# Optimization experiments

Hardware: AMD Instinct MI355X
Metric: run time of the kernel (lower is better)

The kernel has to match this reference:

```python
import jax, jax.numpy as jnp
import numpy as np

PS = 32
D = 256


def setup_inputs() -> dict:
    key = jax.random.key(0)
    ks = jax.random.split(key, 9)
    B, L = 32, 32768
    s_in = 1.0 / np.sqrt(PS)
    s_d = 1.0 / np.sqrt(D)
    return {
        "x": jax.random.normal(ks[0], (B, L), dtype=jnp.float32),
        "W_proj": jax.random.normal(ks[1], (PS, D), dtype=jnp.float32) * s_in,
        "b_proj": jnp.zeros((D,), jnp.float32),
        "W_qkv": jax.random.normal(ks[2], (D, 3 * D), dtype=jnp.float32) * s_d,
        "b_qkv": jnp.zeros((3 * D,), jnp.float32),
        "W_out": jax.random.normal(ks[3], (D, D), dtype=jnp.float32) * s_d,
        "b_out": jnp.zeros((D,), jnp.float32),
        "W_head": jax.random.normal(ks[4], (D, PS), dtype=jnp.float32) * s_d,
        "b_head": jnp.zeros((PS,), jnp.float32),
    }


def reference(x, W_proj, b_proj, W_qkv, b_qkv, W_out, b_out, W_head, b_head):
    B, L = x.shape
    T = L // PS
    # InstanceNorm over full series (torch .std is unbiased -> ddof=1)
    mean = jnp.mean(x, axis=-1, keepdims=True)
    std = jnp.std(x, axis=-1, keepdims=True, ddof=1) + 1e-5
    x_norm = (x - mean) / std
    patches = x_norm.reshape(B, T, PS)
    # Patch embedding
    h = patches @ W_proj + b_proj  # [B, T, D]
    # Single-head causal self-attention (explicit scores, as in source)
    qkv = h @ W_qkv + b_qkv
    q, k, v = jnp.split(qkv, 3, axis=-1)
    scale = 1.0 / jnp.sqrt(jnp.asarray(D, dtype=h.dtype))
    attn = jnp.einsum("btd,bsd->bts", q, k) * scale  # [B, T, T]
    causal = jnp.tril(jnp.ones((T, T), dtype=bool))
    attn = jnp.where(causal, attn, -jnp.inf)
    attn = jax.nn.softmax(attn, axis=-1)
    out = jnp.einsum("bts,bsd->btd", attn, v)
    out = out @ W_out + b_out
    # Prediction head + next-patch MSE loss
    pred = out @ W_head + b_head  # [B, T, PS]
    loss = jnp.mean((pred[:, :-1] - patches[:, 1:]) ** 2)
    return loss
```

## Files before the change

kernel.cpp:

```cpp
#include <hip/hip_runtime.h>
#include <math.h>

#define B_SZ 32
#define L_SZ 32768
#define T_SZ 1024
#define PS_SZ 32
#define D_SZ 256
#define SM_M 10.0f

typedef float f32x4 __attribute__((ext_vector_type(4)));
typedef float f32x16 __attribute__((ext_vector_type(16)));
typedef short s16x8 __attribute__((ext_vector_type(8)));
typedef unsigned short u16x8 __attribute__((ext_vector_type(8)));
typedef unsigned int u32;
typedef unsigned int u32x4 __attribute__((ext_vector_type(4)));

__device__ __forceinline__ unsigned short f2bf(float f) {
  union { float f; unsigned int u; } v; v.f = f;
  unsigned int r = v.u + 0x7FFFu + ((v.u >> 16) & 1u);
  return (unsigned short)(r >> 16);
}

__device__ __forceinline__ void g2l16(const unsigned short* g, unsigned short* l) {
  __builtin_amdgcn_global_load_lds(
      (const __attribute__((address_space(1))) unsigned int*)g,
      (__attribute__((address_space(3))) unsigned int*)l, 16, 0, 0);
}

__global__ __launch_bounds__(256) void prep_kernel(const float* __restrict__ x,
                                                   float* __restrict__ sgpart,
                                                   const float* __restrict__ Wp,
                                                   const float* __restrict__ bp,
                                                   const float* __restrict__ Wq,
                                                   const float* __restrict__ bq,
                                                   const float* __restrict__ Wo,
                                                   const float* __restrict__ bo,
                                                   const float* __restrict__ Wh,
                                                   const float* __restrict__ bh,
                                                   float* __restrict__ Wcb,
                                                   unsigned short* __restrict__ WqT,
                                                   unsigned short* __restrict__ WfT,
                                                   float* __restrict__ bfp,
                                                   unsigned int* __restrict__ total,
                                                   float* __restrict__ lsum) {
  __shared__ float red[8];
  const int g = blockIdx.x, tid = threadIdx.x;
  const int w = tid >> 6, lane = tid & 63;
  if (g < 256) {
    const int b = g >> 3;
    const float* p = x + (size_t)b * L_SZ + (size_t)(g & 7) * 4096;
    float s = 0.f, ss = 0.f;
#pragma unroll
    for (int i = 0; i < 4; ++i) {
      float4 f = ((const float4*)p)[tid + i * 256];
      s += f.x + f.y + f.z + f.w;
      ss += f.x * f.x + f.y * f.y + f.z * f.z + f.w * f.w;
    }
#pragma unroll
    for (int off = 32; off >= 1; off >>= 1) {
      s += __shfl_down(s, off);
      ss += __shfl_down(ss, off);
    }
    if (lane == 0) { red[w] = s; red[4 + w] = ss; }
    __syncthreads();
    if (tid == 0) {
      sgpart[g * 2]     = red[0] + red[1] + red[2] + red[3];
      sgpart[g * 2 + 1] = red[4] + red[5] + red[6] + red[7];
    }
  } else if (g < 388) {
    int idx = (g - 256) * 256 + tid;
    if (idx < 33 * 768) {
      int p = idx / 768, j = idx % 768;
      const float* arow = (p < 32) ? (Wp + p * 256) : bp;
      float acc = (p < 32) ? 0.f : bq[j];
      for (int d = 0; d < 256; ++d) acc += arow[d] * Wq[d * 768 + j];
      if (p < 32) WqT[j * 32 + p] = f2bf(acc);
      else Wcb[j] = acc;
    } else {
      int k = idx - 33 * 768;
      if (k < 8192) {
        int p = k >> 8, d = k & 255;
        float acc = 0.f;
        for (int e = 0; e < 256; ++e) acc += Wo[d * 256 + e] * Wh[e * 32 + p];
        WfT[p * 256 + d] = f2bf(acc);
      } else if (k < 8224) {
        int p = k - 8192;
        float acc = bh[p];
        for (int e = 0; e < 256; ++e) acc += bo[e] * Wh[e * 32 + p];
        bfp[p] = acc;
      }
    }
  } else {
    if (tid == 0) { total[0] = 0u; lsum[0] = 0.f; }
  }
}

__global__ __launch_bounds__(256) void qkv_kernel(const float* __restrict__ x,
                                                  const float* __restrict__ sgpart,
                                                  const unsigned short* __restrict__ WqT,
                                                  const float* __restrict__ Wcb,
                                                  unsigned short* __restrict__ Qb,
                                                  unsigned short* __restrict__ Kb,
                                                  unsigned short* __restrict__ Vtt) {
  __shared__ unsigned short T4[4][8448];
  const int tid = threadIdx.x;
  const int w = tid >> 6, lane = tid & 63;
  const int lo = lane & 15, quad = lane >> 4;
  unsigned short* Tw = T4[w];
  const int mbase = blockIdx.x * 128 + w * 32;
  const int b = mbase >> 10;
  float S = 0.f, SS = 0.f;
#pragma unroll
  for (int i = 0; i < 8; ++i) {
    S += sgpart[(b * 8 + i) * 2];
    SS += sgpart[(b * 8 + i) * 2 + 1];
  }
  const float mean = S * (1.f / (float)L_SZ);
  const float var = (SS - S * mean) * (1.f / (float)(L_SZ - 1));
  const float inv = 1.f / (sqrtf(var) + 1e-5f);
  s16x8 af0, af1;
  {
    float4 a = *(const float4*)&x[(size_t)(mbase + lo) * 32 + quad * 8];
    float4 c = *(const float4*)&x[(size_t)(mbase + lo) * 32 + quad * 8 + 4];
    af0[0] = (short)f2bf((a.x - mean) * inv); af0[1] = (short)f2bf((a.y - mean) * inv);
    af0[2] = (short)f2bf((a.z - mean) * inv); af0[3] = (short)f2bf((a.w - mean) * inv);
    af0[4] = (short)f2bf((c.x - mean) * inv); af0[5] = (short)f2bf((c.y - mean) * inv);
    af0[6] = (short)f2bf((c.z - mean) * inv); af0[7] = (short)f2bf((c.w - mean) * inv);
    float4 d = *(const float4*)&x[(size_t)(mbase + 16 + lo) * 32 + quad * 8];
    float4 e = *(const float4*)&x[(size_t)(mbase + 16 + lo) * 32 + quad * 8 + 4];
    af1[0] = (short)f2bf((d.x - mean) * inv); af1[1] = (short)f2bf((d.y - mean) * inv);
    af1[2] = (short)f2bf((d.z - mean) * inv); af1[3] = (short)f2bf((d.w - mean) * inv);
    af1[4] = (short)f2bf((e.x - mean) * inv); af1[5] = (short)f2bf((e.y - mean) * inv);
    af1[6] = (short)f2bf((e.z - mean) * inv); af1[7] = (short)f2bf((e.w - mean) * inv);
  }
#pragma unroll 4
  for (int nt = 0; nt < 16; ++nt) {
    s16x8 bf = *(const s16x8*)&WqT[(size_t)(nt * 16 + lo) * 32 + quad * 8];
    f32x4 c0 = {0.f, 0.f, 0.f, 0.f}, c1 = {0.f, 0.f, 0.f, 0.f};
    c0 = __builtin_amdgcn_mfma_f32_16x16x32_bf16(af0, bf, c0, 0, 0, 0);
    c1 = __builtin_amdgcn_mfma_f32_16x16x32_bf16(af1, bf, c1, 0, 0, 0);
    const int col = nt * 16 + lo;
    const float bi = Wcb[col];
#pragma unroll
    for (int i = 0; i < 4; ++i) {
      Tw[(quad * 4 + i) * 264 + col]      = f2bf((c0[i] + bi) * 0.0625f);
      Tw[(16 + quad * 4 + i) * 264 + col] = f2bf((c1[i] + bi) * 0.0625f);
    }
  }
#pragma unroll
  for (int it = 0; it < 16; ++it) {
    const int gsub = it * 64 + lane;
    const int row = gsub >> 5, c16 = gsub & 31;
    *(u16x8*)&Qb[(size_t)(mbase + row) * 256 + c16 * 8] =
        *(const u16x8*)&Tw[row * 264 + c16 * 8];
  }
#pragma unroll 4
  for (int nt = 0; nt < 16; ++nt) {
    s16x8 bf = *(const s16x8*)&WqT[(size_t)(256 + nt * 16 + lo) * 32 + quad * 8];
    f32x4 c0 = {0.f, 0.f, 0.f, 0.f}, c1 = {0.f, 0.f, 0.f, 0.f};
    c0 = __builtin_amdgcn_mfma_f32_16x16x32_bf16(af0, bf, c0, 0, 0, 0);
    c1 = __builtin_amdgcn_mfma_f32_16x16x32_bf16(af1, bf, c1, 0, 0, 0);
    const int col = nt * 16 + lo;
    const float bi = Wcb[256 + col];
#pragma unroll
    for (int i = 0; i < 4; ++i) {
      Tw[(quad * 4 + i) * 264 + col]      = f2bf(c0[i] + bi);
      Tw[(16 + quad * 4 + i) * 264 + col] = f2bf(c1[i] + bi);
    }
  }
#pragma unroll
  for (int it = 0; it < 16; ++it) {
    const int gsub = it * 64 + lane;
    const int row = gsub >> 5, c16 = gsub & 31;
    *(u16x8*)&Kb[(size_t)(mbase + row) * 256 + c16 * 8] =
        *(const u16x8*)&Tw[row * 264 + c16 * 8];
  }
#pragma unroll 4
  for (int nt2 = 0; nt2 < 16; ++nt2) {
    s16x8 aw = *(const s16x8*)&WqT[(size_t)(512 + nt2 * 16 + lo) * 32 + quad * 8];
    f32x4 c0 = {0.f, 0.f, 0.f, 0.f}, c1 = {0.f, 0.f, 0.f, 0.f};
    c0 = __builtin_amdgcn_mfma_f32_16x16x32_bf16(aw, af0, c0, 0, 0, 0);
    c1 = __builtin_amdgcn_mfma_f32_16x16x32_bf16(aw, af1, c1, 0, 0, 0);
#pragma unroll
    for (int i = 0; i < 4; ++i) {
      const int d = nt2 * 16 + quad * 4 + i;
      const float bv = Wcb[512 + d];
      Tw[d * 32 + lo]      = f2bf(c0[i] + bv);
      Tw[d * 32 + 16 + lo] = f2bf(c1[i] + bv);
    }
  }
  {
    const int ktq = (mbase >> 5) & 31;
    const size_t vb = ((size_t)b * 32 + ktq) * 8192;
#pragma unroll
    for (int it = 0; it < 16; ++it) {
      const int gsub = it * 64 + lane;
      *(u16x8*)&Vtt[vb + gsub * 8] = *(const u16x8*)&Tw[gsub * 8];
    }
  }
}

__global__ __launch_bounds__(512, 2) void attn_kernel(const unsigned short* __restrict__ Qb,
                                                      const unsigned short* __restrict__ Kb,
                                                      const unsigned short* __restrict__ Vtt,
                                                      const unsigned short* __restrict__ WfT,
                                                      const float* __restrict__ bfp,
                                                      const float* __restrict__ x,
                                                      const float* __restrict__ sgpart,
                                                      float* __restrict__ lsum,
                                                      unsigned int* __restrict__ total,
                                                      float* __restrict__ out) {
  __shared__ unsigned short SMEM[65536];
  __shared__ float redf[8];
  const int g = blockIdx.x;
  const int b = (g & 7) * 4 + ((g >> 3) & 3);
  const int p = g >> 5;
  const int tid = threadIdx.x;
  const int w = tid >> 6, lane = tid & 63;
  const int th = w & 1, dq = w >> 1;
  const int cl = lane & 31, hi = lane >> 5;

  const unsigned short* KbB = Kb + (size_t)b * 262144;
  const unsigned short* VtB = Vtt + (size_t)b * 262144;
  unsigned short* QbM = (unsigned short*)Qb;

  const int c0 = tid, c1 = 512 + tid;
  const int ks0 = (c0 >> 5) * 256 + (((c0 & 31) ^ (c0 >> 5)) * 8);
  const int ks1 = (c1 >> 5) * 256 + (((c1 & 31) ^ (c1 >> 5)) * 8);
  const int vs0 = (c0 >> 2) * 32 + (((c0 & 3) ^ ((c0 >> 4) & 3)) * 8);
  const int vs1 = (c1 >> 2) * 32 + (((c1 & 3) ^ ((c1 >> 4) & 3)) * 8);
  const int kd0 = w * 512, kd1 = 4096 + w * 512;

  auto STAGE = [&](int t) {
    const unsigned short* kg = KbB + (size_t)t * 8192;
    const unsigned short* vg = VtB + (size_t)t * 8192;
    unsigned short* Lb = &SMEM[(t & 3) * 16384];
    g2l16(kg + ks0, Lb + kd0);
    g2l16(kg + ks1, Lb + kd1);
    g2l16(vg + vs0, Lb + 8192 + kd0);
    g2l16(vg + vs1, Lb + 8192 + kd1);
  };

  s16x8 qf[16];
  f32x16 O0, O1;
  float Ol = 0.f;
  const int vsz = (cl >> 2) & 3;
  const int cva = (hi ^ vsz) * 8, cvb = (((2 | hi)) ^ vsz) * 8;

  auto run_phase = [&](int gph) {
    const int nk = 2 * gph + 2;
    const int myti = 2 * gph + th;
    const size_t qrow = ((size_t)b * 1024 + myti * 32 + cl) * 256;
#pragma unroll
    for (int cb = 0; cb < 16; ++cb) qf[cb] = *(const s16x8*)&Qb[qrow + cb * 16 + hi * 8];
#pragma unroll
    for (int i = 0; i < 16; ++i) { O0[i] = 0.f; O1[i] = 0.f; }
    Ol = 0.f;
    const int npre = nk < 3 ? nk : 3;
    for (int s = 0; s < npre; ++s) STAGE(s);
    for (int s = 0; s < nk; ++s) {
      const int rem = nk - 1 - s;
      if (rem >= 2)      asm volatile("s_waitcnt vmcnt(8)" ::: "memory");
      else if (rem == 1) asm volatile("s_waitcnt vmcnt(4)" ::: "memory");
      else               asm volatile("s_waitcnt vmcnt(0)" ::: "memory");
      __builtin_amdgcn_s_barrier();
      __builtin_amdgcn_sched_barrier(0);
      if (s + 3 < nk) STAGE(s + 3);
      if (s <= myti) {
        const unsigned short* Lk = &SMEM[(s & 3) * 16384];
        f32x16 Sx;
#pragma unroll
        for (int i = 0; i < 16; ++i) Sx[i] = 0.f;
#pragma unroll
        for (int cb = 0; cb < 16; ++cb) {
          const int ch = (2 * cb + hi) ^ cl;
          s16x8 kf = *(const s16x8*)&Lk[cl * 256 + ch * 8];
          Sx = __builtin_amdgcn_mfma_f32_32x32x16_bf16(kf, qf[cb], Sx, 0, 0, 0);
        }
        float e[16];
        const bool diag = (s == myti);
#pragma unroll
        for (int r = 0; r < 16; ++r) {
          const int trow = (r & 3) + 8 * (r >> 2) + 4 * hi;
          float ev = __expf(Sx[r] - SM_M);
          if (diag && trow > cl) ev = 0.f;
          e[r] = ev;
          Ol += ev;
        }
        u32 w8[8];
#pragma unroll
        for (int m = 0; m < 8; ++m)
          w8[m] = (u32)f2bf(e[2 * m]) | ((u32)f2bf(e[2 * m + 1]) << 16);
        const u32 r1 = (u32)__shfl_xor((int)(hi ? w8[0] : w8[2]), 32);
        const u32 r2 = (u32)__shfl_xor((int)(hi ? w8[1] : w8[3]), 32);
        const u32 r3 = (u32)__shfl_xor((int)(hi ? w8[4] : w8[6]), 32);
        const u32 r4 = (u32)__shfl_xor((int)(hi ? w8[5] : w8[7]), 32);
        union { u32x4 u; s16x8 s; } p0, p1;
        p0.u[0] = hi ? r1 : w8[0];
        p0.u[1] = hi ? r2 : w8[1];
        p0.u[2] = hi ? w8[2] : r1;
        p0.u[3] = hi ? w8[3] : r2;
        p1.u[0] = hi ? r3 : w8[4];
        p1.u[1] = hi ? r4 : w8[5];
        p1.u[2] = hi ? w8[6] : r3;
        p1.u[3] = hi ? w8[7] : r4;
        const unsigned short* Lv = &SMEM[(s & 3) * 16384 + 8192];
        const int d0 = (dq * 64 + cl) * 32, d1 = (dq * 64 + 32 + cl) * 32;
        s16x8 v0 = *(const s16x8*)&Lv[d0 + cva];
        s16x8 v1 = *(const s16x8*)&Lv[d0 + cvb];
        O0 = __builtin_amdgcn_mfma_f32_32x32x16_bf16(p0.s, v0, O0, 0, 0, 0);
        O0 = __builtin_amdgcn_mfma_f32_32x32x16_bf16(p1.s, v1, O0, 0, 0, 0);
        s16x8 v2 = *(const s16x8*)&Lv[d1 + cva];
        s16x8 v3 = *(const s16x8*)&Lv[d1 + cvb];
        O1 = __builtin_amdgcn_mfma_f32_32x32x16_bf16(p0.s, v2, O1, 0, 0, 0);
        O1 = __builtin_amdgcn_mfma_f32_32x32x16_bf16(p1.s, v3, O1, 0, 0, 0);
      }
    }
    Ol += __shfl_xor(Ol, 32);
  };

  run_phase(p);
  {
    float ivr[16];
#pragma unroll
    for (int r = 0; r < 16; ++r) {
      const int row = (r & 3) + 8 * (r >> 2) + 4 * hi;
      ivr[r] = 1.f / __shfl(Ol, row);
    }
    const size_t obase = ((size_t)b * 1024 + (2 * p + th) * 32) * 256;
#pragma unroll
    for (int r = 0; r < 16; ++r) {
      const int row = (r & 3) + 8 * (r >> 2) + 4 * hi;
      QbM[obase + row * 256 + dq * 64 + cl]      = f2bf(O0[r] * ivr[r]);
      QbM[obase + row * 256 + dq * 64 + 32 + cl] = f2bf(O1[r] * ivr[r]);
    }
  }
  asm volatile("s_waitcnt vmcnt(0)" ::: "memory");
  __builtin_amdgcn_s_barrier();

  run_phase(15 - p);
  __syncthreads();

  unsigned short* OLs = SMEM;
  {
    float ivr[16];
#pragma unroll
    for (int r = 0; r < 16; ++r) {
      const int row = (r & 3) + 8 * (r >> 2) + 4 * hi;
      ivr[r] = 1.f / __shfl(Ol, row);
    }
#pragma unroll
    for (int r = 0; r < 16; ++r) {
      const int row = (r & 3) + 8 * (r >> 2) + 4 * hi;
      OLs[(th * 32 + row) * 264 + dq * 64 + cl]      = f2bf(O0[r] * ivr[r]);
      OLs[(th * 32 + row) * 264 + dq * 64 + 32 + cl] = f2bf(O1[r] * ivr[r]);
    }
  }
  __syncthreads();

  float lacc = 0.f;
  if (w < 4) {
    const int tile = (w == 0) ? 2 * p : (w == 1) ? 2 * p + 1
                   : (w == 2) ? 30 - 2 * p : 31 - 2 * p;
    s16x8 af[16];
    if (w < 2) {
      const size_t abase = ((size_t)b * 1024 + tile * 32 + cl) * 256;
#pragma unroll
      for (int cb = 0; cb < 16; ++cb)
        af[cb] = *(const s16x8*)&QbM[abase + cb * 16 + hi * 8];
    } else {
      const int sub = w - 2;
#pragma unroll
      for (int cb = 0; cb < 16; ++cb)
        af[cb] = *(const s16x8*)&OLs[(sub * 32 + cl) * 264 + cb * 16 + hi * 8];
    }
    f32x16 hacc;
#pragma unroll
    for (int i = 0; i < 16; ++i) hacc[i] = 0.f;
#pragma unroll
    for (int cb = 0; cb < 16; ++cb) {
      s16x8 bfr = *(const s16x8*)&WfT[(size_t)cl * 256 + cb * 16 + hi * 8];
      hacc = __builtin_amdgcn_mfma_f32_32x32x16_bf16(af[cb], bfr, hacc, 0, 0, 0);
    }
    float S_ = 0.f, SS = 0.f;
#pragma unroll
    for (int i = 0; i < 8; ++i) {
      S_ += sgpart[(b * 8 + i) * 2];
      SS += sgpart[(b * 8 + i) * 2 + 1];
    }
    const float mean = S_ * (1.f / (float)L_SZ);
    const float var = (SS - S_ * mean) * (1.f / (float)(L_SZ - 1));
    const float invb = 1.f / (sqrtf(var) + 1e-5f);
    const float ba = bfp[cl];
#pragma unroll
    for (int r = 0; r < 16; ++r) {
      const int row = (r & 3) + 8 * (r >> 2) + 4 * hi;
      const int t = tile * 32 + row;
      if (t < 1023) {
        const float pr = hacc[r] + ba;
        const float tg = (x[(size_t)b * L_SZ + (t + 1) * 32 + cl] - mean) * invb;
        const float d = pr - tg;
        lacc += d * d;
      }
    }
#pragma unroll
    for (int off = 32; off >= 1; off >>= 1) lacc += __shfl_down(lacc, off);
  }
  if (lane == 0) redf[w] = lacc;
  __syncthreads();

  if (tid == 0) {
    atomicAdd(lsum, redf[0] + redf[1] + redf[2] + redf[3]);
    __threadfence();
    unsigned int prev = atomicAdd(total, 1u);
    if (prev == 255u) {
      float tot = atomicAdd(lsum, 0.0f);
      out[0] = tot * (1.f / (float)(B_SZ * (T_SZ - 1) * PS_SZ));
    }
  }
}

extern "C" void kernel_launch(void* const* d_in, const int* in_sizes, int n_in,
                              void* d_out, int out_size, void* d_ws, size_t ws_size,
                              hipStream_t stream) {
  const float* x      = (const float*)d_in[0];
  const float* W_proj = (const float*)d_in[1];
  const float* b_proj = (const float*)d_in[2];
  const float* W_qkv  = (const float*)d_in[3];
  const float* b_qkv  = (const float*)d_in[4];
  const float* W_out  = (const float*)d_in[5];
  const float* b_out  = (const float*)d_in[6];
  const float* W_head = (const float*)d_in[7];
  const float* b_head = (const float*)d_in[8];
  float* out = (float*)d_out;
  char* ws = (char*)d_ws;

  unsigned short* Qb     = (unsigned short*)ws;
  unsigned short* Kb     = (unsigned short*)(ws + (16ull << 20));
  unsigned short* Vtt    = (unsigned short*)(ws + (32ull << 20));
  char* tail = ws + (48ull << 20);
  float*          Wcb    = (float*)tail;
  unsigned short* WqT    = (unsigned short*)(tail + 4096);
  unsigned short* WfT    = (unsigned short*)(tail + 65536);
  float*          bfp    = (float*)(tail + 98304);
  float*          sgpart = (float*)(tail + 102400);
  unsigned int*   total  = (unsigned int*)(tail + 106496);
  float*          lsum   = (float*)(tail + 106496 + 64);

  prep_kernel<<<389, 256, 0, stream>>>(x, sgpart, W_proj, b_proj, W_qkv, b_qkv,
                                       W_out, b_out, W_head, b_head,
                                       Wcb, WqT, WfT, bfp, total, lsum);
  qkv_kernel<<<256, 256, 0, stream>>>(x, sgpart, WqT, Wcb, Qb, Kb, Vtt);
  attn_kernel<<<256, 512, 0, stream>>>(Qb, Kb, Vtt, WfT, bfp, x, sgpart, lsum, total, out);
}
```

Measured before the change: 181.2 us.

## Compute attention scores once per KV tile and share probabilities via LDS

```diff
diff --git a/kernel.cpp b/kernel.cpp
--- a/kernel.cpp
+++ b/kernel.cpp
@@ -13,6 +13,7 @@
 typedef short s16x8 __attribute__((ext_vector_type(8)));
 typedef unsigned short u16x8 __attribute__((ext_vector_type(8)));
 typedef unsigned int u32;
+typedef unsigned int u32x2 __attribute__((ext_vector_type(2)));
 typedef unsigned int u32x4 __attribute__((ext_vector_type(4)));
 
 __device__ __forceinline__ unsigned short f2bf(float f) {
@@ -211,13 +212,15 @@
                                                       unsigned int* __restrict__ total,
                                                       float* __restrict__ out) {
   __shared__ unsigned short SMEM[65536];
+  __shared__ unsigned short Pbuf[2][2][1280];
+  __shared__ float OlL[8][32];
   __shared__ float redf[8];
   const int g = blockIdx.x;
   const int b = (g & 7) * 4 + ((g >> 3) & 3);
   const int p = g >> 5;
   const int tid = threadIdx.x;
   const int w = tid >> 6, lane = tid & 63;
-  const int th = w & 1, dq = w >> 1;
+  const int th = w >> 2, dq = w & 3;
   const int cl = lane & 31, hi = lane >> 5;
 
   const unsigned short* KbB = Kb + (size_t)b * 262144;
@@ -245,115 +248,116 @@
   f32x16 O0, O1;
   float Ol = 0.f;
   const int vsz = (cl >> 2) & 3;
-  const int cva = (hi ^ vsz) * 8, cvb = (((2 | hi)) ^ vsz) * 8;
+  const int cva = (hi ^ vsz) * 8, cvb = ((2 | hi) ^ vsz) * 8;
+
+  auto PRODUCE = [&](int sp, int myti_) {
+    const unsigned short* Lk = &SMEM[(sp & 3) * 16384];
+    f32x16 Sx;
+#pragma unroll
+    for (int i = 0; i < 16; ++i) Sx[i] = 0.f;
+#pragma unroll
+    for (int cb = 0; cb < 16; ++cb) {
+      const int ch = (2 * cb + hi) ^ cl;
+      s16x8 kf = *(const s16x8*)&Lk[cl * 256 + ch * 8];
+      Sx = __builtin_amdgcn_mfma_f32_32x32x16_bf16(kf, qf[cb], Sx, 0, 0, 0);
+    }
+    const bool diag = (sp == myti_);
+    unsigned short* Pd = &Pbuf[th][sp & 1][0];
+#pragma unroll
+    for (int gq = 0; gq < 4; ++gq) {
+      float ev[4];
+#pragma unroll
+      for (int q2 = 0; q2 < 4; ++q2) {
+        const int r = gq * 4 + q2;
+        const int trow = q2 + 8 * gq + 4 * hi;
+        float e = __expf(Sx[r] - SM_M);
+        if (diag && trow > cl) e = 0.f;
+        ev[q2] = e;
+        Ol += e;
+      }
+      u32x2 pr;
+      pr[0] = (u32)f2bf(ev[0]) | ((u32)f2bf(ev[1]) << 16);
+      pr[1] = (u32)f2bf(ev[2]) | ((u32)f2bf(ev[3]) << 16);
+      *(u32x2*)&Pd[cl * 40 + (2 * gq + hi) * 4] = pr;
+    }
+  };
 
   auto run_phase = [&](int gph) {
     const int nk = 2 * gph + 2;
     const int myti = 2 * gph + th;
     const size_t qrow = ((size_t)b * 1024 + myti * 32 + cl) * 256;
 #pragma unroll
-    for (int cb = 0; cb < 16; ++cb) qf[cb] = *(const s16x8*)&Qb[qrow + cb * 16 + hi * 8];
+    for (int cb = 0; cb < 16; ++cb)
+      qf[cb] = *(const s16x8*)&Qb[qrow + cb * 16 + hi * 8];
 #pragma unroll
     for (int i = 0; i < 16; ++i) { O0[i] = 0.f; O1[i] = 0.f; }
     Ol = 0.f;
-    const int npre = nk < 3 ? nk : 3;
-    for (int s = 0; s < npre; ++s) STAGE(s);
+    if (nk >= 3) {
+      STAGE(0); STAGE(1); STAGE(2);
+      asm volatile("s_waitcnt vmcnt(8)" ::: "memory");
+    } else {
+      STAGE(0); STAGE(1);
+      asm volatile("s_waitcnt vmcnt(4)" ::: "memory");
+    }
+    __builtin_amdgcn_s_barrier();
+    if (w == th * 4 + ((2 * th) & 3)) PRODUCE(0, myti);
     for (int s = 0; s < nk; ++s) {
-      const int rem = nk - 1 - s;
-      if (rem >= 2)      asm volatile("s_waitcnt vmcnt(8)" ::: "memory");
-      else if (rem == 1) asm volatile("s_waitcnt vmcnt(4)" ::: "memory");
-      else               asm volatile("s_waitcnt vmcnt(0)" ::: "memory");
+      asm volatile("s_waitcnt lgkmcnt(0)" ::: "memory");
+      if (s + 2 < nk) asm volatile("s_waitcnt vmcnt(4)" ::: "memory");
+      else            asm volatile("s_waitcnt vmcnt(0)" ::: "memory");
       __builtin_amdgcn_s_barrier();
       __builtin_amdgcn_sched_barrier(0);
       if (s + 3 < nk) STAGE(s + 3);
+      if (s + 1 <= myti && w == th * 4 + ((s + 1 + 2 * th) & 3)) PRODUCE(s + 1, myti);
       if (s <= myti) {
-        const unsigned short* Lk = &SMEM[(s & 3) * 16384];
-        f32x16 Sx;
-#pragma unroll
-        for (int i = 0; i < 16; ++i) Sx[i] = 0.f;
-#pragma unroll
-        for (int cb = 0; cb < 16; ++cb) {
-          const int ch = (2 * cb + hi) ^ cl;
-          s16x8 kf = *(const s16x8*)&Lk[cl * 256 + ch * 8];
-          Sx = __builtin_amdgcn_mfma_f32_32x32x16_bf16(kf, qf[cb], Sx, 0, 0, 0);
-        }
-        float e[16];
-        const bool diag = (s == myti);
-#pragma unroll
-        for (int r = 0; r < 16; ++r) {
-          const int trow = (r & 3) + 8 * (r >> 2) + 4 * hi;
-          float ev = __expf(Sx[r] - SM_M);
-          if (diag && trow > cl) ev = 0.f;
-          e[r] = ev;
-          Ol += ev;
-        }
-        u32 w8[8];
-#pragma unroll
-        for (int m = 0; m < 8; ++m)
-          w8[m] = (u32)f2bf(e[2 * m]) | ((u32)f2bf(e[2 * m + 1]) << 16);
-        const u32 r1 = (u32)__shfl_xor((int)(hi ? w8[0] : w8[2]), 32);
-        const u32 r2 = (u32)__shfl_xor((int)(hi ? w8[1] : w8[3]), 32);
-        const u32 r3 = (u32)__shfl_xor((int)(hi ? w8[4] : w8[6]), 32);
-        const u32 r4 = (u32)__shfl_xor((int)(hi ? w8[5] : w8[7]), 32);
-        union { u32x4 u; s16x8 s; } p0, p1;
-        p0.u[0] = hi ? r1 : w8[0];
-        p0.u[1] = hi ? r2 : w8[1];
-        p0.u[2] = hi ? w8[2] : r1;
-        p0.u[3] = hi ? w8[3] : r2;
-        p1.u[0] = hi ? r3 : w8[4];
-        p1.u[1] = hi ? r4 : w8[5];
-        p1.u[2] = hi ? w8[6] : r3;
-        p1.u[3] = hi ? w8[7] : r4;
+        const unsigned short* Pp = &Pbuf[th][s & 1][0];
+        s16x8 pa = *(const s16x8*)&Pp[cl * 40 + 8 * hi];
+        s16x8 pb = *(const s16x8*)&Pp[cl * 40 + 16 + 8 * hi];
         const unsigned short* Lv = &SMEM[(s & 3) * 16384 + 8192];
-        const int d0 = (dq * 64 + cl) * 32, d1 = (dq * 64 + 32 + cl) * 32;
+        const int d0 = (dq * 64 + cl) * 32;
         s16x8 v0 = *(const s16x8*)&Lv[d0 + cva];
         s16x8 v1 = *(const s16x8*)&Lv[d0 + cvb];
-        O0 = __builtin_amdgcn_mfma_f32_32x32x16_bf16(p0.s, v0, O0, 0, 0, 0);
-        O0 = __builtin_amdgcn_mfma_f32_32x32x16_bf16(p1.s, v1, O0, 0, 0, 0);
-        s16x8 v2 = *(const s16x8*)&Lv[d1 + cva];
-        s16x8 v3 = *(const s16x8*)&Lv[d1 + cvb];
-        O1 = __builtin_amdgcn_mfma_f32_32x32x16_bf16(p0.s, v2, O1, 0, 0, 0);
-        O1 = __builtin_amdgcn_mfma_f32_32x32x16_bf16(p1.s, v3, O1, 0, 0, 0);
+        O0 = __builtin_amdgcn_mfma_f32_32x32x16_bf16(pa, v0, O0, 0, 0, 0);
+        O0 = __builtin_amdgcn_mfma_f32_32x32x16_bf16(pb, v1, O0, 0, 0, 0);
+        s16x8 v2 = *(const s16x8*)&Lv[d0 + 1024 + cva];
+        s16x8 v3 = *(const s16x8*)&Lv[d0 + 1024 + cvb];
+        O1 = __builtin_amdgcn_mfma_f32_32x32x16_bf16(pa, v2, O1, 0, 0, 0);
+        O1 = __builtin_amdgcn_mfma_f32_32x32x16_bf16(pb, v3, O1, 0, 0, 0);
       }
     }
     Ol += __shfl_xor(Ol, 32);
   };
 
   run_phase(p);
+  if (hi == 0) OlL[w][cl] = Ol;
+  __syncthreads();
   {
-    float ivr[16];
+    const float dsum = OlL[th * 4][cl] + OlL[th * 4 + 1][cl] +
+                       OlL[th * 4 + 2][cl] + OlL[th * 4 + 3][cl];
+    const size_t obase = ((size_t)b * 1024 + (2 * p + th) * 32) * 256;
 #pragma unroll
     for (int r = 0; r < 16; ++r) {
       const int row = (r & 3) + 8 * (r >> 2) + 4 * hi;
-      ivr[r] = 1.f / __shfl(Ol, row);
-    }
-    const size_t obase = ((size_t)b * 1024 + (2 * p + th) * 32) * 256;
+      const float iv = 1.f / __shfl(dsum, row);
+      QbM[obase + row * 256 + dq * 64 + cl]      = f2bf(O0[r] * iv);
+      QbM[obase + row * 256 + dq * 64 + 32 + cl] = f2bf(O1[r] * iv);
+    }
+  }
+  __syncthreads();
+
+  run_phase(15 - p);
+  if (hi == 0) OlL[w][cl] = Ol;
+  __syncthreads();
+  unsigned short* OLs = SMEM;
+  {
+    const float dsum = OlL[th * 4][cl] + OlL[th * 4 + 1][cl] +
+                       OlL[th * 4 + 2][cl] + OlL[th * 4 + 3][cl];
 #pragma unroll
     for (int r = 0; r < 16; ++r) {
       const int row = (r & 3) + 8 * (r >> 2) + 4 * hi;
-      QbM[obase + row * 256 + dq * 64 + cl]      = f2bf(O0[r] * ivr[r]);
-      QbM[obase + row * 256 + dq * 64 + 32 + cl] = f2bf(O1[r] * ivr[r]);
-    }
-  }
-  asm volatile("s_waitcnt vmcnt(0)" ::: "memory");
-  __builtin_amdgcn_s_barrier();
-
-  run_phase(15 - p);
-  __syncthreads();
-
-  unsigned short* OLs = SMEM;
-  {
-    float ivr[16];
-#pragma unroll
-    for (int r = 0; r < 16; ++r) {
-      const int row = (r & 3) + 8 * (r >> 2) + 4 * hi;
-      ivr[r] = 1.f / __shfl(Ol, row);
-    }
-#pragma unroll
-    for (int r = 0; r < 16; ++r) {
-      const int row = (r & 3) + 8 * (r >> 2) + 4 * hi;
-      OLs[(th * 32 + row) * 264 + dq * 64 + cl]      = f2bf(O0[r] * ivr[r]);
-      OLs[(th * 32 + row) * 264 + dq * 64 + 32 + cl] = f2bf(O1[r] * ivr[r]);
+      const float iv = 1.f / __shfl(dsum, row);
+      OLs[(th * 32 + row) * 264 + dq * 64 + cl]      = f2bf(O0[r] * iv);
+      OLs[(th * 32 + row) * 264 + dq * 64 + 32 + cl] = f2bf(O1[r] * iv);
     }
   }
   __syncthreads();
```

Result: faster. 171.9 us (-5.2%).
